# Performance work log

Measured on AMD Instinct MI355X. Metric: run time of the kernel, lower is better.

Reference implementation:

```python
import jax, jax.numpy as jnp
import numpy as np
from jax import lax


def setup_inputs() -> dict:
    key = jax.random.key(0)
    k1, k2, k3 = jax.random.split(key, 3)
    B, F, L = 16384, 1024, 3
    x = jax.random.normal(k1, (B, F), dtype=jnp.float32)
    # xavier_uniform on [F,1]: bound = sqrt(6/(F+1))
    bound = float(np.sqrt(6.0 / (F + 1)))
    kernels = jax.random.uniform(k2, (L, F, 1), dtype=jnp.float32, minval=-bound, maxval=bound)
    bias = jax.random.uniform(k3, (L, F, 1), dtype=jnp.float32, minval=-bound, maxval=bound)
    return {"x": x, "kernels": kernels, "bias": bias}


def reference(x, kernels, bias):
    # DCN vector cross: xl_{i+1} = x0 * (xl . w_i) + b_i + xl
    x0 = x  # [B, F]

    def step(xl, wb):
        w, b = wb  # w: [F,1], b: [F,1]
        s = xl @ w[:, 0]                     # [B]  (xl^T w per batch row)
        xl_new = x0 * s[:, None] + b[:, 0] + xl  # [B, F]
        return xl_new, None

    xl, _ = lax.scan(step, x0, (kernels, bias))
    return xl
```

## Files before the change

### kernel.cpp

```cpp
#include <hip/hip_runtime.h>


constexpr int B = 16384;
constexpr int F = 1024;
constexpr int WAVES = 4;
constexpr int RPW = 2;
constexpr int ROWS_PER_BLOCK = WAVES * RPW;
constexpr int BLOCK = 64 * WAVES;

typedef float v4f __attribute__((ext_vector_type(4)));

__global__ __launch_bounds__(BLOCK) void prep_kernel(
    const float* __restrict__ kernels,
    const float* __restrict__ bias,
    float* __restrict__ ws)
{
    const int tid = threadIdx.x;
    const v4f* w1v = (const v4f*)(kernels + F);
    const v4f* w2v = (const v4f*)(kernels + 2 * F);
    const v4f* b0v = (const v4f*)(bias);
    const v4f* b1v = (const v4f*)(bias + F);
    const v4f* b2v = (const v4f*)(bias + 2 * F);

    const v4f B0 = b0v[tid];
    const v4f B1 = b1v[tid];
    const v4f B2 = b2v[tid];
    v4f bs;
    bs.x = B0.x + B1.x + B2.x;
    bs.y = B0.y + B1.y + B2.y;
    bs.z = B0.z + B1.z + B2.z;
    bs.w = B0.w + B1.w + B2.w;
    ((v4f*)(ws + 4))[tid] = bs;

    if (tid < 64) {
        float t01 = 0.f, t02 = 0.f, t12 = 0.f;
#pragma unroll
        for (int c = 0; c < 4; ++c) {
            const int i = c * 64 + tid;
            const v4f w1 = w1v[i];
            const v4f w2 = w2v[i];
            const v4f b0 = b0v[i];
            const v4f b1 = b1v[i];
            t01 = fmaf(b0.x, w1.x, t01); t01 = fmaf(b0.y, w1.y, t01);
            t01 = fmaf(b0.z, w1.z, t01); t01 = fmaf(b0.w, w1.w, t01);
            t02 = fmaf(b0.x, w2.x, t02); t02 = fmaf(b0.y, w2.y, t02);
            t02 = fmaf(b0.z, w2.z, t02); t02 = fmaf(b0.w, w2.w, t02);
            t12 = fmaf(b1.x, w2.x, t12); t12 = fmaf(b1.y, w2.y, t12);
            t12 = fmaf(b1.z, w2.z, t12); t12 = fmaf(b1.w, w2.w, t12);
        }
#pragma unroll
        for (int off = 32; off >= 1; off >>= 1) {
            t01 += __shfl_xor(t01, off, 64);
            t02 += __shfl_xor(t02, off, 64);
            t12 += __shfl_xor(t12, off, 64);
        }
        if (tid == 0) { ws[0] = t01; ws[1] = t02; ws[2] = t12; }
    }
}

__global__ __launch_bounds__(BLOCK) void cross_layer_kernel(
    const float* __restrict__ x,
    const float* __restrict__ kernels,
    const float* __restrict__ ws,
    float* __restrict__ out)
{
    const int lane = threadIdx.x & 63;
    const int wave = threadIdx.x >> 6;
    const int row0 = blockIdx.x * ROWS_PER_BLOCK + wave * RPW;

    const v4f* w0v = (const v4f*)(kernels);
    const v4f* w1v = (const v4f*)(kernels + F);
    const v4f* w2v = (const v4f*)(kernels + 2 * F);
    const v4f* bsv = (const v4f*)(ws + 4);

    v4f xr[RPW][4];
#pragma unroll
    for (int r = 0; r < RPW; ++r) {
        const v4f* xrow = (const v4f*)(x + (size_t)(row0 + r) * F);
#pragma unroll
        for (int c = 0; c < 4; ++c) xr[r][c] = xrow[c * 64 + lane];
    }

    const float t01  = ws[0];
    const float tsum = ws[1] + ws[2];

    float d00 = 0.f, d01 = 0.f, d02 = 0.f;
    float d10 = 0.f, d11 = 0.f, d12 = 0.f;
#pragma unroll
    for (int c = 0; c < 4; ++c) {
        const int i = c * 64 + lane;
        const v4f w0 = w0v[i];
        const v4f w1 = w1v[i];
        const v4f w2 = w2v[i];
        const v4f a = xr[0][c];
        const v4f b = xr[1][c];
        d00 = fmaf(a.x, w0.x, d00); d00 = fmaf(a.y, w0.y, d00);
        d00 = fmaf(a.z, w0.z, d00); d00 = fmaf(a.w, w0.w, d00);
        d01 = fmaf(a.x, w1.x, d01); d01 = fmaf(a.y, w1.y, d01);
        d01 = fmaf(a.z, w1.z, d01); d01 = fmaf(a.w, w1.w, d01);
        d02 = fmaf(a.x, w2.x, d02); d02 = fmaf(a.y, w2.y, d02);
        d02 = fmaf(a.z, w2.z, d02); d02 = fmaf(a.w, w2.w, d02);
        d10 = fmaf(b.x, w0.x, d10); d10 = fmaf(b.y, w0.y, d10);
        d10 = fmaf(b.z, w0.z, d10); d10 = fmaf(b.w, w0.w, d10);
        d11 = fmaf(b.x, w1.x, d11); d11 = fmaf(b.y, w1.y, d11);
        d11 = fmaf(b.z, w1.z, d11); d11 = fmaf(b.w, w1.w, d11);
        d12 = fmaf(b.x, w2.x, d12); d12 = fmaf(b.y, w2.y, d12);
        d12 = fmaf(b.z, w2.z, d12); d12 = fmaf(b.w, w2.w, d12);
    }

#pragma unroll
    for (int off = 32; off >= 1; off >>= 1) {
        d00 += __shfl_xor(d00, off, 64);
        d01 += __shfl_xor(d01, off, 64);
        d02 += __shfl_xor(d02, off, 64);
        d10 += __shfl_xor(d10, off, 64);
        d11 += __shfl_xor(d11, off, 64);
        d12 += __shfl_xor(d12, off, 64);
    }

    float S0, S1;
    {
        const float a1 = 1.f + d00;
        const float s1 = fmaf(a1, d01, t01);
        const float a2 = a1 + s1;
        const float s2 = fmaf(a2, d02, tsum);
        S0 = a2 + s2;
    }
    {
        const float a1 = 1.f + d10;
        const float s1 = fmaf(a1, d11, t01);
        const float a2 = a1 + s1;
        const float s2 = fmaf(a2, d12, tsum);
        S1 = a2 + s2;
    }

    v4f* orow0 = (v4f*)(out + (size_t)row0 * F);
    v4f* orow1 = (v4f*)(out + (size_t)(row0 + 1) * F);
#pragma unroll
    for (int c = 0; c < 4; ++c) {
        const int i = c * 64 + lane;
        const v4f bs = bsv[i];
        v4f o0, o1;
        o0.x = fmaf(xr[0][c].x, S0, bs.x);
        o0.y = fmaf(xr[0][c].y, S0, bs.y);
        o0.z = fmaf(xr[0][c].z, S0, bs.z);
        o0.w = fmaf(xr[0][c].w, S0, bs.w);
        o1.x = fmaf(xr[1][c].x, S1, bs.x);
        o1.y = fmaf(xr[1][c].y, S1, bs.y);
        o1.z = fmaf(xr[1][c].z, S1, bs.z);
        o1.w = fmaf(xr[1][c].w, S1, bs.w);
        __builtin_nontemporal_store(o0, &orow0[i]);
        __builtin_nontemporal_store(o1, &orow1[i]);
    }
}

extern "C" void kernel_launch(void* const* d_in, const int* in_sizes, int n_in,
                              void* d_out, int out_size, void* d_ws, size_t ws_size,
                              hipStream_t stream) {
    const float* x       = (const float*)d_in[0];
    const float* kernels = (const float*)d_in[1];
    const float* bias    = (const float*)d_in[2];
    float* out           = (float*)d_out;
    float* ws            = (float*)d_ws;

    prep_kernel<<<dim3(1), dim3(BLOCK), 0, stream>>>(kernels, bias, ws);
    cross_layer_kernel<<<dim3(B / ROWS_PER_BLOCK), dim3(BLOCK), 0, stream>>>(
        x, kernels, ws, out);
}
```

Measured before the change: 114.7 us.

## Fuse bias-precompute into main kernel, computing per-block via LDS

Removes the separate single-block prep kernel and recomputes the bias sum and bias-weight dot products inside every block of the main kernel, distributing the work across waves and sharing results through LDS with a block barrier. This is meant to eliminate one kernel launch and the serial dependency between the two launches. In exchange every block redundantly reads the bias and weight vectors, which are L2-resident, and all waves now wait at a __syncthreads.

Result: faster. 112.0 us (-2.4%).

```diff
diff --git a/kernel.cpp b/kernel.cpp
--- a/kernel.cpp
+++ b/kernel.cpp
@@ -10,60 +10,15 @@
 
 typedef float v4f __attribute__((ext_vector_type(4)));
 
-__global__ __launch_bounds__(BLOCK) void prep_kernel(
-    const float* __restrict__ kernels,
-    const float* __restrict__ bias,
-    float* __restrict__ ws)
-{
-    const int tid = threadIdx.x;
-    const v4f* w1v = (const v4f*)(kernels + F);
-    const v4f* w2v = (const v4f*)(kernels + 2 * F);
-    const v4f* b0v = (const v4f*)(bias);
-    const v4f* b1v = (const v4f*)(bias + F);
-    const v4f* b2v = (const v4f*)(bias + 2 * F);
-
-    const v4f B0 = b0v[tid];
-    const v4f B1 = b1v[tid];
-    const v4f B2 = b2v[tid];
-    v4f bs;
-    bs.x = B0.x + B1.x + B2.x;
-    bs.y = B0.y + B1.y + B2.y;
-    bs.z = B0.z + B1.z + B2.z;
-    bs.w = B0.w + B1.w + B2.w;
-    ((v4f*)(ws + 4))[tid] = bs;
-
-    if (tid < 64) {
-        float t01 = 0.f, t02 = 0.f, t12 = 0.f;
-#pragma unroll
-        for (int c = 0; c < 4; ++c) {
-            const int i = c * 64 + tid;
-            const v4f w1 = w1v[i];
-            const v4f w2 = w2v[i];
-            const v4f b0 = b0v[i];
-            const v4f b1 = b1v[i];
-            t01 = fmaf(b0.x, w1.x, t01); t01 = fmaf(b0.y, w1.y, t01);
-            t01 = fmaf(b0.z, w1.z, t01); t01 = fmaf(b0.w, w1.w, t01);
-            t02 = fmaf(b0.x, w2.x, t02); t02 = fmaf(b0.y, w2.y, t02);
-            t02 = fmaf(b0.z, w2.z, t02); t02 = fmaf(b0.w, w2.w, t02);
-            t12 = fmaf(b1.x, w2.x, t12); t12 = fmaf(b1.y, w2.y, t12);
-            t12 = fmaf(b1.z, w2.z, t12); t12 = fmaf(b1.w, w2.w, t12);
-        }
-#pragma unroll
-        for (int off = 32; off >= 1; off >>= 1) {
-            t01 += __shfl_xor(t01, off, 64);
-            t02 += __shfl_xor(t02, off, 64);
-            t12 += __shfl_xor(t12, off, 64);
-        }
-        if (tid == 0) { ws[0] = t01; ws[1] = t02; ws[2] = t12; }
-    }
-}
-
 __global__ __launch_bounds__(BLOCK) void cross_layer_kernel(
     const float* __restrict__ x,
     const float* __restrict__ kernels,
-    const float* __restrict__ ws,
+    const float* __restrict__ bias,
     float* __restrict__ out)
 {
+    __shared__ v4f   bs_lds[F / 4];
+    __shared__ float t_lds[3];
+
     const int lane = threadIdx.x & 63;
     const int wave = threadIdx.x >> 6;
     const int row0 = blockIdx.x * ROWS_PER_BLOCK + wave * RPW;
@@ -71,7 +26,9 @@
     const v4f* w0v = (const v4f*)(kernels);
     const v4f* w1v = (const v4f*)(kernels + F);
     const v4f* w2v = (const v4f*)(kernels + 2 * F);
-    const v4f* bsv = (const v4f*)(ws + 4);
+    const v4f* b0v = (const v4f*)(bias);
+    const v4f* b1v = (const v4f*)(bias + F);
+    const v4f* b2v = (const v4f*)(bias + 2 * F);
 
     v4f xr[RPW][4];
 #pragma unroll
@@ -81,8 +38,14 @@
         for (int c = 0; c < 4; ++c) xr[r][c] = xrow[c * 64 + lane];
     }
 
-    const float t01  = ws[0];
-    const float tsum = ws[1] + ws[2];
+    if (wave >= 2) {
+        const int t2 = threadIdx.x - 128;
+#pragma unroll
+        for (int k = 0; k < 2; ++k) {
+            const int i = t2 + k * 128;
+            bs_lds[i] = b0v[i] + b1v[i] + b2v[i];
+        }
+    }
 
     float d00 = 0.f, d01 = 0.f, d02 = 0.f;
     float d10 = 0.f, d11 = 0.f, d12 = 0.f;
@@ -108,15 +71,70 @@
         d12 = fmaf(b.z, w2.z, d12); d12 = fmaf(b.w, w2.w, d12);
     }
 
+    float e0 = 0.f, e1 = 0.f;
+    if (wave == 0) {
 #pragma unroll
-    for (int off = 32; off >= 1; off >>= 1) {
-        d00 += __shfl_xor(d00, off, 64);
-        d01 += __shfl_xor(d01, off, 64);
-        d02 += __shfl_xor(d02, off, 64);
-        d10 += __shfl_xor(d10, off, 64);
-        d11 += __shfl_xor(d11, off, 64);
-        d12 += __shfl_xor(d12, off, 64);
+        for (int c = 0; c < 4; ++c) {
+            const int i = c * 64 + lane;
+            const v4f b0 = b0v[i];
+            const v4f w1 = w1v[i];
+            const v4f w2 = w2v[i];
+            e0 = fmaf(b0.x, w1.x, e0); e0 = fmaf(b0.y, w1.y, e0);
+            e0 = fmaf(b0.z, w1.z, e0); e0 = fmaf(b0.w, w1.w, e0);
+            e1 = fmaf(b0.x, w2.x, e1); e1 = fmaf(b0.y, w2.y, e1);
+            e1 = fmaf(b0.z, w2.z, e1); e1 = fmaf(b0.w, w2.w, e1);
+        }
+    } else if (wave == 1) {
+#pragma unroll
+        for (int c = 0; c < 4; ++c) {
+            const int i = c * 64 + lane;
+            const v4f b1 = b1v[i];
+            const v4f w2 = w2v[i];
+            e0 = fmaf(b1.x, w2.x, e0); e0 = fmaf(b1.y, w2.y, e0);
+            e0 = fmaf(b1.z, w2.z, e0); e0 = fmaf(b1.w, w2.w, e0);
+        }
     }
+
+    if (wave == 0) {
+#pragma unroll
+        for (int off = 32; off >= 1; off >>= 1) {
+            d00 += __shfl_xor(d00, off, 64);
+            d01 += __shfl_xor(d01, off, 64);
+            d02 += __shfl_xor(d02, off, 64);
+            d10 += __shfl_xor(d10, off, 64);
+            d11 += __shfl_xor(d11, off, 64);
+            d12 += __shfl_xor(d12, off, 64);
+            e0  += __shfl_xor(e0,  off, 64);
+            e1  += __shfl_xor(e1,  off, 64);
+        }
+        if (lane == 0) { t_lds[0] = e0; t_lds[1] = e1; }
+    } else if (wave == 1) {
+#pragma unroll
+        for (int off = 32; off >= 1; off >>= 1) {
+            d00 += __shfl_xor(d00, off, 64);
+            d01 += __shfl_xor(d01, off, 64);
+            d02 += __shfl_xor(d02, off, 64);
+            d10 += __shfl_xor(d10, off, 64);
+            d11 += __shfl_xor(d11, off, 64);
+            d12 += __shfl_xor(d12, off, 64);
+            e0  += __shfl_xor(e0,  off, 64);
+        }
+        if (lane == 0) { t_lds[2] = e0; }
+    } else {
+#pragma unroll
+        for (int off = 32; off >= 1; off >>= 1) {
+            d00 += __shfl_xor(d00, off, 64);
+            d01 += __shfl_xor(d01, off, 64);
+            d02 += __shfl_xor(d02, off, 64);
+            d10 += __shfl_xor(d10, off, 64);
+            d11 += __shfl_xor(d11, off, 64);
+            d12 += __shfl_xor(d12, off, 64);
+        }
+    }
+
+    __syncthreads();
+    const float t01  = t_lds[0];
+    const float tsum = t_lds[1] + t_lds[2];
 
     float S0, S1;
     {
@@ -139,7 +157,7 @@
 #pragma unroll
     for (int c = 0; c < 4; ++c) {
         const int i = c * 64 + lane;
-        const v4f bs = bsv[i];
+        const v4f bs = bs_lds[i];
         v4f o0, o1;
         o0.x = fmaf(xr[0][c].x, S0, bs.x);
         o0.y = fmaf(xr[0][c].y, S0, bs.y);
@@ -161,9 +179,7 @@
     const float* kernels = (const float*)d_in[1];
     const float* bias    = (const float*)d_in[2];
     float* out           = (float*)d_out;
-    float* ws            = (float*)d_ws;
 
-    prep_kernel<<<dim3(1), dim3(BLOCK), 0, stream>>>(kernels, bias, ws);
     cross_layer_kernel<<<dim3(B / ROWS_PER_BLOCK), dim3(BLOCK), 0, stream>>>(
-        x, kernels, ws, out);
+        x, kernels, bias, out);
 }
```
